# Kernel optimization log

Measured on AMD Instinct MI355X. Metric: run time of the kernel, lower is better.

Reference implementation:

```python
import jax, jax.numpy as jnp
import numpy as np

R = 0.2          # stable-distribution hash bucket width
TABLE_SIZE = 2   # hash table size (buckets)
M = 5            # number of appended ALSH transform dims
EPS = 1e-12


def conv2d(x, W, b, pad):
    out = jax.lax.conv_general_dilated(
        x, W, window_strides=(1, 1), padding=[(pad, pad), (pad, pad)],
        dimension_numbers=('NCHW', 'OIHW', 'NCHW'))
    return out + b[None, :, None, None]


def maxpool2(x):
    return jax.lax.reduce_window(x, -jnp.inf, jax.lax.max,
                                 (1, 1, 2, 2), (1, 1, 2, 2), 'VALID')


def alsh_mask(x, W, a, c):
    """ALSH filter selection: hash P(kernels) and Q(query) with a stable
    distribution hash h(v)=floor((a.v+b)/r) mod table_size; active filters
    are those landing in the query's bucket. Returns [B, Cout] 0/1 mask.
    Multiplying conv output by this mask == gather active filters then
    zero_fill_missing back to full channel count."""
    Cout, Cin, kH, kW = W.shape
    Kf = W.reshape(Cout, -1)                       # [Cout, Cin*kH*kW]
    norms = jnp.linalg.norm(Kf, axis=1)
    Kn = Kf / (jnp.max(norms) + EPS)               # scale so all norms <= 1
    n = jnp.linalg.norm(Kn, axis=1, keepdims=True)
    # P transform: append norm^2, norm^4, ..., norm^(2^M)
    powers = jnp.concatenate([n ** (2 ** (i + 1)) for i in range(M)], axis=1)
    P = jnp.concatenate([Kn, powers], axis=1)      # [Cout, d+M]
    kh = jnp.mod(jnp.floor((P @ a + c[0]) / R), TABLE_SIZE)  # [Cout]
    # query vector: per-sample channel means broadcast over kernel support
    cm = x.mean(axis=(2, 3))                       # [B, Cin]
    q = jnp.repeat(cm, kH * kW, axis=1)            # [B, Cin*kH*kW] (cin,kh,kw order)
    qn = q / (jnp.linalg.norm(q, axis=1, keepdims=True) + EPS)
    # Q transform: append M halves
    Qv = jnp.concatenate([qn, jnp.full((q.shape[0], M), 0.5, q.dtype)], axis=1)
    qh = jnp.mod(jnp.floor((Qv @ a + c[0]) / R), TABLE_SIZE)  # [B]
    return (kh[None, :] == qh[:, None]).astype(x.dtype)       # [B, Cout]


def setup_inputs() -> dict:
    key = jax.random.key(0)
    ks = jax.random.split(key, 16)
    u = lambda k, s: jax.random.uniform(k, s, jnp.float32, 0.0, R)
    n = lambda k, s, sc=0.1: jax.random.normal(k, s, jnp.float32) * sc
    return {
        'x': jax.random.normal(ks[0], (4096, 3, 32, 32), jnp.float32),
        'W1': n(ks[1], (16, 3, 5, 5)), 'b1': n(ks[2], (16,)),
        'a1': jax.random.normal(ks[3], (80,), jnp.float32), 'c1': u(ks[4], (1,)),
        'W2': n(ks[5], (20, 16, 5, 5)), 'b2': n(ks[6], (20,)),
        'a2': jax.random.normal(ks[7], (405,), jnp.float32), 'c2': u(ks[8], (1,)),
        'W3': n(ks[9], (20, 20, 5, 5)), 'b3': n(ks[10], (20,)),
        'a3': jax.random.normal(ks[11], (505,), jnp.float32), 'c3': u(ks[12], (1,)),
        'Wo': n(ks[13], (10, 320)), 'bo': n(ks[14], (10,)),
    }


def reference(x, W1, b1, a1, c1, W2, b2, a2, c2, W3, b3, a3, c3, Wo, bo):
    m1 = alsh_mask(x, W1, a1, c1)
    h = jax.nn.relu(conv2d(x, W1, b1, 2)) * m1[:, :, None, None]
    h = maxpool2(h)                                # [B,16,16,16]
    m2 = alsh_mask(h, W2, a2, c2)
    h = jax.nn.relu(conv2d(h, W2, b2, 2)) * m2[:, :, None, None]
    h = maxpool2(h)                                # [B,20,8,8]
    m3 = alsh_mask(h, W3, a3, c3)
    h = jax.nn.relu(conv2d(h, W3, b3, 2)) * m3[:, :, None, None]
    # zero_fill_missing -> identity here: inactive channels already zero
    h = maxpool2(h)                                # [B,20,4,4]
    flat = h.reshape(h.shape[0], -1)               # [B,320]
    return flat @ Wo.T + bo
```

## Files before the change

kernel.cpp:

```cpp
#include <hip/hip_runtime.h>
#include <hip/hip_bf16.h>

#define EPSV 1e-12
#define RHASH 0.2

__device__ __forceinline__ int fmod2(double t) {
    return (int)(((long long)floor(t)) & 1LL);
}

__device__ __forceinline__ void load_row6(const float* base, float* r) {
    float2 a0 = *(const float2*)(base);
    float2 a1 = *(const float2*)(base + 2);
    float2 a2 = *(const float2*)(base + 4);
    r[0] = a0.x; r[1] = a0.y; r[2] = a1.x; r[3] = a1.y; r[4] = a2.x; r[5] = a2.y;
}

__device__ __forceinline__ void load_row12(const float* base, float* r) {
    #pragma unroll
    for (int j = 0; j < 6; ++j) *(float2*)&r[2 * j] = *(const float2*)(base + 2 * j);
}

#define FMA4(c,kx,w) { float wg=(w); \
  acc[c][0]=fmaf(wg,cur[kx],acc[c][0]); acc[c][1]=fmaf(wg,cur[(kx)+1],acc[c][1]); \
  acc[c][2]=fmaf(wg,nxt[kx],acc[c][2]); acc[c][3]=fmaf(wg,nxt[(kx)+1],acc[c][3]); }

__device__ void layer_setup(const float* W, const float* a, double cval,
                            int Co, int Ci, int* kh, double* asum, double* qc,
                            double* s_norm, float* Wbuf, float* abuf)
{
    const int t = threadIdx.x;
    const int w = t >> 6, ln = t & 63;
    const int D = Ci * 25;
    for (int i = t; i < Co * D; i += 256) Wbuf[i] = W[i];
    for (int i = t; i < D + 5; i += 256) abuf[i] = a[i];
    __syncthreads();
    for (int co = w; co < Co; co += 4) {
        double s = 0;
        for (int j = ln; j < D; j += 64) { double x = (double)Wbuf[co * D + j]; s += x * x; }
        #pragma unroll
        for (int off = 32; off; off >>= 1) s += __shfl_xor(s, off);
        if (ln == 0) s_norm[co] = sqrt(s);
    }
    __syncthreads();
    if (t == 0) {
        double mx = 0;
        for (int i = 0; i < Co; ++i) mx = fmax(mx, s_norm[i]);
        s_norm[23] = 1.0 / (mx + EPSV);
    }
    __syncthreads();
    double scale = s_norm[23];
    for (int co = w; co < Co; co += 4) {
        double dp = 0;
        for (int j = ln; j < D; j += 64) dp += (double)Wbuf[co * D + j] * (double)abuf[j];
        #pragma unroll
        for (int off = 32; off; off >>= 1) dp += __shfl_xor(dp, off);
        if (ln == 0) {
            dp *= scale;
            double n = s_norm[co] * scale;
            double p = n * n;
            for (int m = 0; m < 5; ++m) { dp += p * (double)abuf[D + m]; p *= p; }
            kh[co] = fmod2((dp + cval) / RHASH);
        }
    }
    if (t >= 64 && t < 64 + Ci) {
        int c = t - 64;
        double s = 0;
        for (int j = 0; j < 25; ++j) s += (double)abuf[c * 25 + j];
        asum[c] = s;
    }
    if (t == 128) {
        double s = 0;
        for (int m = 0; m < 5; ++m) s += (double)abuf[D + m];
        *qc = 0.5 * s + cval;
    }
    __syncthreads();
}

__global__ __launch_bounds__(256) void prep_kernel(
    const float* W1, const float* a1, const float* c1,
    const float* W2, const float* a2, const float* c2,
    const float* W3, const float* a3, const float* c3,
    double* dmeta, int* imeta,
    float* Wp1, float* Wp2, float* Wp3)
{
    __shared__ float Wbuf[10000];
    __shared__ float abuf[512];
    __shared__ double s_norm[24];
    const int blk = blockIdx.x;
    if (blk == 0) {
        layer_setup(W1, a1, (double)c1[0], 16, 3,  imeta + 0,  dmeta + 0,  dmeta + 39, s_norm, Wbuf, abuf);
    } else if (blk == 1) {
        layer_setup(W2, a2, (double)c2[0], 20, 16, imeta + 16, dmeta + 3,  dmeta + 40, s_norm, Wbuf, abuf);
    } else if (blk == 2) {
        layer_setup(W3, a3, (double)c3[0], 20, 20, imeta + 36, dmeta + 19, dmeta + 41, s_norm, Wbuf, abuf);
    } else {
        int i = (blk - 3) * 256 + threadIdx.x;
        if (i < 1200) {
            int co = i & 15, r = i >> 4;
            int kx = r % 5, r2 = r / 5, ky = r2 % 5, ci = r2 / 5;
            Wp1[i] = W1[co * 75 + ci * 25 + ky * 5 + kx];
        } else if (i < 1200 + 8960) {
            int k = i - 1200;
            int j = k % 28, r = k / 28;
            int cog = r % 4, r2 = r / 4, ky = r2 % 5, ci = r2 / 5;
            Wp2[k] = (j < 25) ? W2[(cog * 5 + j / 5) * 400 + ci * 25 + ky * 5 + (j % 5)] : 0.f;
        } else if (i < 1200 + 8960 + 11200) {
            int k = i - 10160;
            int j = k % 28, r = k / 28;
            int cog = r % 4, r2 = r / 4, ky = r2 % 5, ci = r2 / 5;
            Wp3[k] = (j < 25) ? W3[(cog * 5 + j / 5) * 500 + ci * 25 + ky * 5 + (j % 5)] : 0.f;
        }
    }
}

__global__ __launch_bounds__(256) void conv1_kernel(
    const float* __restrict__ x, const float* __restrict__ Wp1,
    const float* __restrict__ b1, const int* __restrict__ kh1,
    const double* __restrict__ dmeta, float* __restrict__ h1,
    int* __restrict__ qh2)
{
    __shared__ float xs[3][36][38];
    __shared__ float Ws[1200];
    __shared__ double s_red[3][4];
    __shared__ double s_ch[16][4];

    const int b = blockIdx.x, t = threadIdx.x;
    const int w = t >> 6, ln = t & 63;

    for (int i = t; i < 3 * 36 * 38; i += 256) (&xs[0][0][0])[i] = 0.f;
    for (int i = t; i < 600; i += 256) ((float2*)Ws)[i] = ((const float2*)Wp1)[i];
    __syncthreads();

    const float2* xb2 = (const float2*)(x + (size_t)b * 3072);
    double psum[3] = {0, 0, 0};
    #pragma unroll
    for (int j = 0; j < 6; ++j) {
        int i = t + 256 * j;
        int rem = i & 511, row = rem >> 4, col2 = rem & 15;
        float2 v = xb2[i];
        *(float2*)&xs[j >> 1][row + 2][col2 * 2 + 2] = v;
        psum[j >> 1] += (double)v.x + (double)v.y;
    }
    #pragma unroll
    for (int c = 0; c < 3; ++c) {
        double s = psum[c];
        #pragma unroll
        for (int off = 32; off; off >>= 1) s += __shfl_xor(s, off);
        if (ln == 0) s_red[c][w] = s;
    }
    __syncthreads();

    double dp = 0, nn = 0;
    #pragma unroll
    for (int c = 0; c < 3; ++c) {
        double cm = (s_red[c][0] + s_red[c][1] + s_red[c][2] + s_red[c][3]) * (1.0 / 1024.0);
        dp += cm * dmeta[c]; nn += cm * cm;
    }
    const int qh = fmod2((dp / (5.0 * sqrt(nn) + EPSV) + dmeta[39]) / RHASH);

    const int cog = ln >> 4;
    const int py = 4 * w + ((ln >> 2) & 3), pxg = ln & 3;
    const int y0 = 2 * py, x0 = 8 * pxg;

    float accA[4][8], accB[4][8];
    #pragma unroll
    for (int c = 0; c < 4; ++c) {
        float bb = b1[cog * 4 + c];
        #pragma unroll
        for (int k = 0; k < 8; ++k) { accA[c][k] = bb; accB[c][k] = bb; }
    }

    #pragma unroll
    for (int ci = 0; ci < 3; ++ci) {
        float ra[12], rb[12];
        load_row12(&xs[ci][y0][x0],     ra);
        load_row12(&xs[ci][y0 + 1][x0], rb);
        #pragma unroll
        for (int ky = 0; ky < 5; ++ky) {
            const float4* wq = (const float4*)&Ws[((ci * 5 + ky) * 5) * 16 + cog * 4];
            #pragma unroll
            for (int kx = 0; kx < 5; ++kx) {
                float4 wv = wq[kx * 4];
                { float wg = wv.x;
                  #pragma unroll
                  for (int k = 0; k < 8; ++k) { accA[0][k] = fmaf(wg, ra[k + kx], accA[0][k]);
                                                accB[0][k] = fmaf(wg, rb[k + kx], accB[0][k]); } }
                { float wg = wv.y;
                  #pragma unroll
                  for (int k = 0; k < 8; ++k) { accA[1][k] = fmaf(wg, ra[k + kx], accA[1][k]);
                                                accB[1][k] = fmaf(wg, rb[k + kx], accB[1][k]); } }
                { float wg = wv.z;
                  #pragma unroll
                  for (int k = 0; k < 8; ++k) { accA[2][k] = fmaf(wg, ra[k + kx], accA[2][k]);
                                                accB[2][k] = fmaf(wg, rb[k + kx], accB[2][k]); } }
                { float wg = wv.w;
                  #pragma unroll
                  for (int k = 0; k < 8; ++k) { accA[3][k] = fmaf(wg, ra[k + kx], accA[3][k]);
                                                accB[3][k] = fmaf(wg, rb[k + kx], accB[3][k]); } }
            }
            if (ky < 4) {
                #pragma unroll
                for (int j = 0; j < 12; ++j) ra[j] = rb[j];
                load_row12(&xs[ci][y0 + ky + 2][x0], rb);
            }
        }
    }

    float* hb = h1 + (size_t)b * 4096 + py * 16 + pxg * 4;
    double csum[4];
    #pragma unroll
    for (int c = 0; c < 4; ++c) {
        int co = cog * 4 + c;
        float mask = (kh1[co] == qh) ? 1.f : 0.f;
        float v0 = fmaxf(fmaxf(accA[c][0], accA[c][1]), fmaxf(accB[c][0], accB[c][1]));
        float v1 = fmaxf(fmaxf(accA[c][2], accA[c][3]), fmaxf(accB[c][2], accB[c][3]));
        float v2 = fmaxf(fmaxf(accA[c][4], accA[c][5]), fmaxf(accB[c][4], accB[c][5]));
        float v3 = fmaxf(fmaxf(accA[c][6], accA[c][7]), fmaxf(accB[c][6], accB[c][7]));
        v0 = fmaxf(v0, 0.f) * mask; v1 = fmaxf(v1, 0.f) * mask;
        v2 = fmaxf(v2, 0.f) * mask; v3 = fmaxf(v3, 0.f) * mask;
        *(float4*)(hb + co * 256) = make_float4(v0, v1, v2, v3);
        csum[c] = (double)v0 + (double)v1 + (double)v2 + (double)v3;
    }
    #pragma unroll
    for (int c = 0; c < 4; ++c) {
        double s = csum[c];
        s += __shfl_xor(s, 8); s += __shfl_xor(s, 4);
        s += __shfl_xor(s, 2); s += __shfl_xor(s, 1);
        if ((ln & 15) == 0) s_ch[cog * 4 + c][w] = s;
    }
    __syncthreads();
    if (t == 0) {
        double dp2 = 0, nn2 = 0;
        #pragma unroll
        for (int c = 0; c < 16; ++c) {
            double cm = (s_ch[c][0] + s_ch[c][1] + s_ch[c][2] + s_ch[c][3]) * (1.0 / 256.0);
            dp2 += cm * dmeta[3 + c]; nn2 += cm * cm;
        }
        qh2[b] = fmod2((dp2 / (5.0 * sqrt(nn2) + EPSV) + dmeta[40]) / RHASH);
    }
}

#define C2_XLOAD(CH, RX) { \
    _Pragma("unroll") \
    for (int j = 0; j < 8; ++j) { \
        int i = t + 256 * j, si = i >> 9, rem = i & 511, cil = rem >> 7, rr = rem & 127; \
        RX[j] = (b0 + si < B) ? ((const float2*)h1)[(size_t)(b0 + si) * 2048 + ((CH) * 4 + cil) * 128 + rr] \
                              : make_float2(0.f, 0.f); \
    } }

#define C2_XCOMMIT(RX) { \
    _Pragma("unroll") \
    for (int j = 0; j < 8; ++j) { \
        int i = t + 256 * j, si = i >> 9, rem = i & 511, cil = rem >> 7, rr = rem & 127; \
        int p2 = rr * 2, row = p2 >> 4, col = p2 & 15; \
        *(float2*)&xs[si][cil][row + 2][col + 2] = RX[j]; \
    } }

__global__ __launch_bounds__(256) void conv2_kernel(
    const float* __restrict__ h1, const float* __restrict__ Wp2,
    const float* __restrict__ b2, const int* __restrict__ kh2,
    const int* __restrict__ qh2, const double* __restrict__ dmeta,
    float* __restrict__ h2, int* __restrict__ qh3, int B)
{
    __shared__ float xs[4][4][20][22];
    __shared__ float Ws[2240];
    __shared__ double s_ch[4][20];

    const int b0 = blockIdx.x * 4, t = threadIdx.x;
    const int s = t >> 6, l = t & 63;
    const int cog = l >> 4, pos = l & 15;
    const int py = pos >> 1, pxg = pos & 1;
    const int b = b0 + s;

    for (int i = t; i < 4 * 4 * 20 * 22; i += 256) (&xs[0][0][0][0])[i] = 0.f;

    const int qh = (b < B) ? qh2[b] : 0;
    float accA[5][8], accB[5][8];
    #pragma unroll
    for (int c = 0; c < 5; ++c) {
        float bb = b2[cog * 5 + c];
        #pragma unroll
        for (int k = 0; k < 8; ++k) { accA[c][k] = bb; accB[c][k] = bb; }
    }

    float2 rx[8];
    C2_XLOAD(0, rx);
    __syncthreads();

    for (int ch = 0; ch < 4; ++ch) {
        for (int i = t; i < 1120; i += 256)
            ((float2*)Ws)[i] = ((const float2*)(Wp2 + ch * 2240))[i];
        C2_XCOMMIT(rx);
        __syncthreads();
        if (ch < 3) C2_XLOAD(ch + 1, rx);

        for (int cil = 0; cil < 4; ++cil) {
            float ra[12], rb[12];
            load_row12(&xs[s][cil][2 * py][8 * pxg],     ra);
            load_row12(&xs[s][cil][2 * py + 1][8 * pxg], rb);
            #pragma unroll
            for (int ky = 0; ky < 5; ++ky) {
                float wv[28];
                const float4* wp = (const float4*)&Ws[((cil * 5 + ky) * 4 + cog) * 28];
                *(float4*)&wv[0]  = wp[0];
                *(float4*)&wv[4]  = wp[1];
                *(float4*)&wv[8]  = wp[2];
                *(float4*)&wv[12] = wp[3];
                *(float4*)&wv[16] = wp[4];
                *(float4*)&wv[20] = wp[5];
                *(float4*)&wv[24] = wp[6];
                #pragma unroll
                for (int c = 0; c < 5; ++c) {
                    #pragma unroll
                    for (int kx = 0; kx < 5; ++kx) {
                        float wg = wv[c * 5 + kx];
                        #pragma unroll
                        for (int k = 0; k < 8; ++k) {
                            accA[c][k] = fmaf(wg, ra[k + kx], accA[c][k]);
                            accB[c][k] = fmaf(wg, rb[k + kx], accB[c][k]);
                        }
                    }
                }
                if (ky < 4) {
                    #pragma unroll
                    for (int j = 0; j < 12; ++j) ra[j] = rb[j];
                    load_row12(&xs[s][cil][2 * py + ky + 2][8 * pxg], rb);
                }
            }
        }
        __syncthreads();
    }

    float* ob = h2 + (size_t)b * 1280 + py * 8 + pxg * 4;
    double csum[5];
    #pragma unroll
    for (int c = 0; c < 5; ++c) {
        int co = cog * 5 + c;
        float mask = (kh2[co] == qh) ? 1.f : 0.f;
        float v0 = fmaxf(fmaxf(accA[c][0], accA[c][1]), fmaxf(accB[c][0], accB[c][1]));
        float v1 = fmaxf(fmaxf(accA[c][2], accA[c][3]), fmaxf(accB[c][2], accB[c][3]));
        float v2 = fmaxf(fmaxf(accA[c][4], accA[c][5]), fmaxf(accB[c][4], accB[c][5]));
        float v3 = fmaxf(fmaxf(accA[c][6], accA[c][7]), fmaxf(accB[c][6], accB[c][7]));
        v0 = fmaxf(v0, 0.f) * mask; v1 = fmaxf(v1, 0.f) * mask;
        v2 = fmaxf(v2, 0.f) * mask; v3 = fmaxf(v3, 0.f) * mask;
        if (b < B) *(float4*)(ob + co * 64) = make_float4(v0, v1, v2, v3);
        csum[c] = (double)v0 + (double)v1 + (double)v2 + (double)v3;
    }
    #pragma unroll
    for (int c = 0; c < 5; ++c) {
        double sv = csum[c];
        sv += __shfl_xor(sv, 8); sv += __shfl_xor(sv, 4);
        sv += __shfl_xor(sv, 2); sv += __shfl_xor(sv, 1);
        if (pos == 0) s_ch[s][cog * 5 + c] = sv;
    }
    __syncthreads();
    if (l == 0 && b < B) {
        double dp2 = 0, nn2 = 0;
        #pragma unroll
        for (int c = 0; c < 20; ++c) {
            double cm = s_ch[s][c] * (1.0 / 64.0);
            dp2 += cm * dmeta[19 + c]; nn2 += cm * cm;
        }
        qh3[b] = fmod2((dp2 / (5.0 * sqrt(nn2) + EPSV) + dmeta[41]) / RHASH);
    }
}

#define C3_WLOAD(CH, RW) { \
    _Pragma("unroll") \
    for (int j = 0; j < 6; ++j) { \
        int i = t + 256 * j; \
        if (i < 1400) RW[j] = ((const float2*)(Wp3 + (CH) * 2800))[i]; \
    } }

#define C3_WCOMMIT(RW) { \
    _Pragma("unroll") \
    for (int j = 0; j < 6; ++j) { \
        int i = t + 256 * j; \
        if (i < 1400) ((float2*)Ws)[i] = RW[j]; \
    } }

#define C3_XLOAD(CH, RX) { \
    _Pragma("unroll") \
    for (int j = 0; j < 3; ++j) { \
        int i = t + 256 * j; \
        if (i < 640) { \
            int ss = i / 160, r = i - ss * 160, ci = r >> 5, rr = r & 31; \
            RX[j] = (b0 + ss < B) ? ((const float2*)(h2 + (size_t)(b0 + ss) * 1280 + ((CH) * 5 + ci) * 64))[rr] \
                                  : make_float2(0.f, 0.f); \
        } \
    } }

#define C3_XCOMMIT(RX) { \
    _Pragma("unroll") \
    for (int j = 0; j < 3; ++j) { \
        int i = t + 256 * j; \
        if (i < 640) { \
            int ss = i / 160, r = i - ss * 160, ci = r >> 5, rr = r & 31, p2 = rr * 2; \
            *(float2*)&xs[ss][ci][(p2 >> 3) + 2][(p2 & 7) + 2] = RX[j]; \
        } \
    } }

__global__ __launch_bounds__(256) void conv3_kernel(
    const float* __restrict__ h2, const float* __restrict__ Wp3,
    const float* __restrict__ b3, const int* __restrict__ kh3,
    const int* __restrict__ qh3,
    const float* __restrict__ Wo, const float* __restrict__ bo,
    float* __restrict__ out, int B)
{
    __shared__ float xs[4][5][12][12];
    __shared__ float Ws[2800];
    __shared__ float flat[4][320];

    const int b0 = blockIdx.x * 4, t = threadIdx.x;
    const int s = t >> 6, q0 = t & 63, cog = q0 >> 4, pos = q0 & 15;
    const int py = pos >> 2, px = pos & 3;
    const int y0 = 2 * py, x0 = 2 * px;
    const int b = b0 + s;

    for (int i = t; i < 4 * 5 * 144; i += 256) (&xs[0][0][0][0])[i] = 0.f;

    const int qh = (b < B) ? qh3[b] : 0;
    float acc[5][4];
    #pragma unroll
    for (int c = 0; c < 5; ++c) {
        float bb = b3[cog * 5 + c];
        acc[c][0] = bb; acc[c][1] = bb; acc[c][2] = bb; acc[c][3] = bb;
    }

    float2 rw[6], rx[3];
    C3_WLOAD(0, rw);
    C3_XLOAD(0, rx);

    for (int ch = 0; ch < 4; ++ch) {
        C3_WCOMMIT(rw);
        C3_XCOMMIT(rx);
        __syncthreads();
        if (ch < 3) { C3_WLOAD(ch + 1, rw); C3_XLOAD(ch + 1, rx); }

        #pragma unroll
        for (int ci = 0; ci < 5; ++ci) {
            float cur[6], nxt[6];
            load_row6(&xs[s][ci][y0][x0], cur);
            load_row6(&xs[s][ci][y0 + 1][x0], nxt);
            #pragma unroll
            for (int ky = 0; ky < 5; ++ky) {
                const float* wrow = &Ws[((ci * 5 + ky) * 4 + cog) * 28];
                const float4* wq = (const float4*)wrow;
                float4 q;
                q = wq[0]; FMA4(0, 0, q.x) FMA4(0, 1, q.y) FMA4(0, 2, q.z) FMA4(0, 3, q.w)
                q = wq[1]; FMA4(0, 4, q.x) FMA4(1, 0, q.y) FMA4(1, 1, q.z) FMA4(1, 2, q.w)
                q = wq[2]; FMA4(1, 3, q.x) FMA4(1, 4, q.y) FMA4(2, 0, q.z) FMA4(2, 1, q.w)
                q = wq[3]; FMA4(2, 2, q.x) FMA4(2, 3, q.y) FMA4(2, 4, q.z) FMA4(3, 0, q.w)
                q = wq[4]; FMA4(3, 1, q.x) FMA4(3, 2, q.y) FMA4(3, 3, q.z) FMA4(3, 4, q.w)
                q = wq[5]; FMA4(4, 0, q.x) FMA4(4, 1, q.y) FMA4(4, 2, q.z) FMA4(4, 3, q.w)
                FMA4(4, 4, wrow[24])
                if (ky < 4) {
                    #pragma unroll
                    for (int j = 0; j < 6; ++j) cur[j] = nxt[j];
                    load_row6(&xs[s][ci][y0 + ky + 2][x0], nxt);
                }
            }
        }
        __syncthreads();
    }

    #pragma unroll
    for (int c = 0; c < 5; ++c) {
        int co = cog * 5 + c;
        float m = fmaxf(fmaxf(acc[c][0], acc[c][1]), fmaxf(acc[c][2], acc[c][3]));
        flat[s][co * 16 + pos] = fmaxf(m, 0.f) * ((kh3[co] == qh) ? 1.f : 0.f);
    }
    __syncthreads();

    if (t < 160) {
        const int g = t >> 2, qq = t & 3;
        const int ss = g / 10, o = g - ss * 10;
        float a = 0.f;
        const float* wr = Wo + o * 320;
        for (int k = qq; k < 320; k += 4) a = fmaf(flat[ss][k], wr[k], a);
        a += __shfl_xor(a, 1);
        a += __shfl_xor(a, 2);
        if (qq == 0 && b0 + ss < B) out[(size_t)(b0 + ss) * 10 + o] = a + bo[o];
    }
}

extern "C" void kernel_launch(void* const* d_in, const int* in_sizes, int n_in,
                              void* d_out, int out_size, void* d_ws, size_t ws_size,
                              hipStream_t stream)
{
    const float* x  = (const float*)d_in[0];
    const float* W1 = (const float*)d_in[1];
    const float* b1 = (const float*)d_in[2];
    const float* a1 = (const float*)d_in[3];
    const float* c1 = (const float*)d_in[4];
    const float* W2 = (const float*)d_in[5];
    const float* b2 = (const float*)d_in[6];
    const float* a2 = (const float*)d_in[7];
    const float* c2 = (const float*)d_in[8];
    const float* W3 = (const float*)d_in[9];
    const float* b3 = (const float*)d_in[10];
    const float* a3 = (const float*)d_in[11];
    const float* c3 = (const float*)d_in[12];
    const float* Wo = (const float*)d_in[13];
    const float* bo = (const float*)d_in[14];
    float* out = (float*)d_out;

    const int B = in_sizes[0] / 3072;

    float* h1  = (float*)d_ws;
    float* h2  = h1 + (size_t)B * 4096;
    float* Wp1 = h2 + (size_t)B * 1280;
    float* Wp2 = Wp1 + 1200;
    float* Wp3 = Wp2 + 8960;
    double* dmeta = (double*)(Wp3 + 11200);
    int* imeta = (int*)(dmeta + 42);
    int* qh2 = imeta + 56;
    int* qh3 = qh2 + B;

    prep_kernel<<<87, 256, 0, stream>>>(W1, a1, c1, W2, a2, c2, W3, a3, c3,
                                        dmeta, imeta, Wp1, Wp2, Wp3);
    conv1_kernel<<<B, 256, 0, stream>>>(x, Wp1, b1, imeta, dmeta, h1, qh2);
    conv2_kernel<<<(B + 3) / 4, 256, 0, stream>>>(h1, Wp2, b2, imeta + 16, qh2, dmeta, h2, qh3, B);
    conv3_kernel<<<(B + 3) / 4, 256, 0, stream>>>(h2, Wp3, b3, imeta + 36, qh3, Wo, bo, out, B);
}
```

Before: 468.9 us.

## Widen conv3 to 8 samples per block and zero only padding halos

conv3 now runs 512 threads per block on 8 samples. Each weight chunk loaded to shared memory is reused across twice as many samples, and input channels are staged in 2 chunks of 10 instead of 4 chunks of 5, so there are fewer sync rounds. The flat buffer reuses the xs shared memory, and both conv1 and conv3 write zeros only to the halo border instead of clearing the whole tile. conv1 also issues its global input loads before the weight copy so their latency overlaps. The larger shared footprint (about 68KB) and 512-thread blocks may lower occupancy and halve the number of conv3 blocks.

```diff
diff --git a/kernel.cpp b/kernel.cpp
--- a/kernel.cpp
+++ b/kernel.cpp
@@ -127,19 +127,27 @@
     const int b = blockIdx.x, t = threadIdx.x;
     const int w = t >> 6, ln = t & 63;
 
-    for (int i = t; i < 3 * 36 * 38; i += 256) (&xs[0][0][0])[i] = 0.f;
+    const float2* xb2 = (const float2*)(x + (size_t)b * 3072);
+    float2 rxv[6];
+    #pragma unroll
+    for (int j = 0; j < 6; ++j) rxv[j] = xb2[t + 256 * j];
+
     for (int i = t; i < 600; i += 256) ((float2*)Ws)[i] = ((const float2*)Wp1)[i];
-    __syncthreads();
-
-    const float2* xb2 = (const float2*)(x + (size_t)b * 3072);
+
+    for (int i = t; i < 1032; i += 256) {
+        int ci = i / 344, r = i - ci * 344;
+        int row, col;
+        if (r < 152) { int rr = r / 38; col = r - rr * 38; row = (rr < 2) ? rr : rr + 32; }
+        else { int q = r - 152; row = 2 + q / 6; int cq = q - (q / 6) * 6; col = (cq < 2) ? cq : cq + 32; }
+        xs[ci][row][col] = 0.f;
+    }
+
     double psum[3] = {0, 0, 0};
     #pragma unroll
     for (int j = 0; j < 6; ++j) {
-        int i = t + 256 * j;
-        int rem = i & 511, row = rem >> 4, col2 = rem & 15;
-        float2 v = xb2[i];
-        *(float2*)&xs[j >> 1][row + 2][col2 * 2 + 2] = v;
-        psum[j >> 1] += (double)v.x + (double)v.y;
+        int i = t + 256 * j, rem = i & 511, row = rem >> 4, col2 = rem & 15;
+        *(float2*)&xs[j >> 1][row + 2][col2 * 2 + 2] = rxv[j];
+        psum[j >> 1] += (double)rxv[j].x + (double)rxv[j].y;
     }
     #pragma unroll
     for (int c = 0; c < 3; ++c) {
@@ -365,60 +373,78 @@
     }
 }
 
-#define C3_WLOAD(CH, RW) { \
+#define C3B_WLOAD(CH, RW) { \
     _Pragma("unroll") \
     for (int j = 0; j < 6; ++j) { \
-        int i = t + 256 * j; \
-        if (i < 1400) RW[j] = ((const float2*)(Wp3 + (CH) * 2800))[i]; \
-    } }
-
-#define C3_WCOMMIT(RW) { \
+        int i = t + 512 * j; \
+        if (i < 2800) RW[j] = ((const float2*)(Wp3 + (CH) * 5600))[i]; \
+    } }
+
+#define C3B_WCOMMIT(RW) { \
     _Pragma("unroll") \
     for (int j = 0; j < 6; ++j) { \
-        int i = t + 256 * j; \
-        if (i < 1400) ((float2*)Ws)[i] = RW[j]; \
-    } }
-
-#define C3_XLOAD(CH, RX) { \
+        int i = t + 512 * j; \
+        if (i < 2800) ((float2*)Ws)[i] = RW[j]; \
+    } }
+
+#define C3B_XLOAD(CH, RX) { \
     _Pragma("unroll") \
-    for (int j = 0; j < 3; ++j) { \
-        int i = t + 256 * j; \
-        if (i < 640) { \
-            int ss = i / 160, r = i - ss * 160, ci = r >> 5, rr = r & 31; \
-            RX[j] = (b0 + ss < B) ? ((const float2*)(h2 + (size_t)(b0 + ss) * 1280 + ((CH) * 5 + ci) * 64))[rr] \
-                                  : make_float2(0.f, 0.f); \
+    for (int j = 0; j < 5; ++j) { \
+        int i = t + 512 * j; \
+        int ss = i / 320, r = i - ss * 320, ci = r >> 5, rr = r & 31; \
+        RX[j] = (b0 + ss < B) ? ((const float2*)(h2 + (size_t)(b0 + ss) * 1280 + ((CH) * 10 + ci) * 64))[rr] \
+                              : make_float2(0.f, 0.f); \
+    } }
+
+#define C3B_XCOMMIT(RX) { \
+    _Pragma("unroll") \
+    for (int j = 0; j < 5; ++j) { \
+        int i = t + 512 * j; \
+        int ss = i / 320, r = i - ss * 320, ci = r >> 5, rr = r & 31, p2 = rr * 2; \
+        *(float2*)&xs[ss][ci][(p2 >> 3) + 2][(p2 & 7) + 2] = RX[j]; \
+    } }
+
+#define C3B_COMPUTE { \
+    for (int ci = 0; ci < 10; ++ci) { \
+        float cur[6], nxt[6]; \
+        load_row6(&xs[s][ci][y0][x0], cur); \
+        load_row6(&xs[s][ci][y0 + 1][x0], nxt); \
+        _Pragma("unroll") \
+        for (int ky = 0; ky < 5; ++ky) { \
+            const float* wrow = &Ws[((ci * 5 + ky) * 4 + cog) * 28]; \
+            const float4* wq = (const float4*)wrow; \
+            float4 q; \
+            q = wq[0]; FMA4(0, 0, q.x) FMA4(0, 1, q.y) FMA4(0, 2, q.z) FMA4(0, 3, q.w) \
+            q = wq[1]; FMA4(0, 4, q.x) FMA4(1, 0, q.y) FMA4(1, 1, q.z) FMA4(1, 2, q.w) \
+            q = wq[2]; FMA4(1, 3, q.x) FMA4(1, 4, q.y) FMA4(2, 0, q.z) FMA4(2, 1, q.w) \
+            q = wq[3]; FMA4(2, 2, q.x) FMA4(2, 3, q.y) FMA4(2, 4, q.z) FMA4(3, 0, q.w) \
+            q = wq[4]; FMA4(3, 1, q.x) FMA4(3, 2, q.y) FMA4(3, 3, q.z) FMA4(3, 4, q.w) \
+            q = wq[5]; FMA4(4, 0, q.x) FMA4(4, 1, q.y) FMA4(4, 2, q.z) FMA4(4, 3, q.w) \
+            FMA4(4, 4, wrow[24]) \
+            if (ky < 4) { \
+                _Pragma("unroll") \
+                for (int j = 0; j < 6; ++j) cur[j] = nxt[j]; \
+                load_row6(&xs[s][ci][y0 + ky + 2][x0], nxt); \
+            } \
         } \
     } }
 
-#define C3_XCOMMIT(RX) { \
-    _Pragma("unroll") \
-    for (int j = 0; j < 3; ++j) { \
-        int i = t + 256 * j; \
-        if (i < 640) { \
-            int ss = i / 160, r = i - ss * 160, ci = r >> 5, rr = r & 31, p2 = rr * 2; \
-            *(float2*)&xs[ss][ci][(p2 >> 3) + 2][(p2 & 7) + 2] = RX[j]; \
-        } \
-    } }
-
-__global__ __launch_bounds__(256) void conv3_kernel(
+__global__ __launch_bounds__(512) void conv3_kernel(
     const float* __restrict__ h2, const float* __restrict__ Wp3,
     const float* __restrict__ b3, const int* __restrict__ kh3,
     const int* __restrict__ qh3,
     const float* __restrict__ Wo, const float* __restrict__ bo,
     float* __restrict__ out, int B)
 {
-    __shared__ float xs[4][5][12][12];
-    __shared__ float Ws[2800];
-    __shared__ float flat[4][320];
-
-    const int b0 = blockIdx.x * 4, t = threadIdx.x;
+    __shared__ float xs[8][10][12][12];
+    __shared__ float Ws[5600];
+
+    const int b0 = blockIdx.x * 8, t = threadIdx.x;
     const int s = t >> 6, q0 = t & 63, cog = q0 >> 4, pos = q0 & 15;
     const int py = pos >> 2, px = pos & 3;
     const int y0 = 2 * py, x0 = 2 * px;
     const int b = b0 + s;
 
-    for (int i = t; i < 4 * 5 * 144; i += 256) (&xs[0][0][0][0])[i] = 0.f;
-
     const int qh = (b < B) ? qh3[b] : 0;
     float acc[5][4];
     #pragma unroll
@@ -427,57 +453,47 @@
         acc[c][0] = bb; acc[c][1] = bb; acc[c][2] = bb; acc[c][3] = bb;
     }
 
-    float2 rw[6], rx[3];
-    C3_WLOAD(0, rw);
-    C3_XLOAD(0, rx);
-
-    for (int ch = 0; ch < 4; ++ch) {
-        C3_WCOMMIT(rw);
-        C3_XCOMMIT(rx);
-        __syncthreads();
-        if (ch < 3) { C3_WLOAD(ch + 1, rw); C3_XLOAD(ch + 1, rx); }
-
-        #pragma unroll
-        for (int ci = 0; ci < 5; ++ci) {
-            float cur[6], nxt[6];
-            load_row6(&xs[s][ci][y0][x0], cur);
-            load_row6(&xs[s][ci][y0 + 1][x0], nxt);
-            #pragma unroll
-            for (int ky = 0; ky < 5; ++ky) {
-                const float* wrow = &Ws[((ci * 5 + ky) * 4 + cog) * 28];
-                const float4* wq = (const float4*)wrow;
-                float4 q;
-                q = wq[0]; FMA4(0, 0, q.x) FMA4(0, 1, q.y) FMA4(0, 2, q.z) FMA4(0, 3, q.w)
-                q = wq[1]; FMA4(0, 4, q.x) FMA4(1, 0, q.y) FMA4(1, 1, q.z) FMA4(1, 2, q.w)
-                q = wq[2]; FMA4(1, 3, q.x) FMA4(1, 4, q.y) FMA4(2, 0, q.z) FMA4(2, 1, q.w)
-                q = wq[3]; FMA4(2, 2, q.x) FMA4(2, 3, q.y) FMA4(2, 4, q.z) FMA4(3, 0, q.w)
-                q = wq[4]; FMA4(3, 1, q.x) FMA4(3, 2, q.y) FMA4(3, 3, q.z) FMA4(3, 4, q.w)
-                q = wq[5]; FMA4(4, 0, q.x) FMA4(4, 1, q.y) FMA4(4, 2, q.z) FMA4(4, 3, q.w)
-                FMA4(4, 4, wrow[24])
-                if (ky < 4) {
-                    #pragma unroll
-                    for (int j = 0; j < 6; ++j) cur[j] = nxt[j];
-                    load_row6(&xs[s][ci][y0 + ky + 2][x0], nxt);
-                }
-            }
-        }
-        __syncthreads();
-    }
-
+    float2 rw[6], rx[5];
+    C3B_WLOAD(0, rw);
+    C3B_XLOAD(0, rx);
+
+    for (int i = t; i < 6400; i += 512) {
+        int tile = i / 80, r = i - tile * 80;
+        int ss = tile / 10, ci = tile - ss * 10;
+        int row, col;
+        if (r < 48) { int rr = r / 12; col = r - rr * 12; row = (rr < 2) ? rr : rr + 8; }
+        else { int q = r - 48; row = 2 + (q >> 2); int cq = q & 3; col = (cq < 2) ? cq : cq + 8; }
+        xs[ss][ci][row][col] = 0.f;
+    }
+    C3B_WCOMMIT(rw);
+    C3B_XCOMMIT(rx);
+    __syncthreads();
+
+    C3B_WLOAD(1, rw);
+    C3B_XLOAD(1, rx);
+    C3B_COMPUTE
+    __syncthreads();
+    C3B_WCOMMIT(rw);
+    C3B_XCOMMIT(rx);
+    __syncthreads();
+    C3B_COMPUTE
+    __syncthreads();
+
+    float* flat = &xs[0][0][0][0];
     #pragma unroll
     for (int c = 0; c < 5; ++c) {
         int co = cog * 5 + c;
         float m = fmaxf(fmaxf(acc[c][0], acc[c][1]), fmaxf(acc[c][2], acc[c][3]));
-        flat[s][co * 16 + pos] = fmaxf(m, 0.f) * ((kh3[co] == qh) ? 1.f : 0.f);
-    }
-    __syncthreads();
-
-    if (t < 160) {
+        flat[s * 320 + co * 16 + pos] = fmaxf(m, 0.f) * ((kh3[co] == qh) ? 1.f : 0.f);
+    }
+    __syncthreads();
+
+    if (t < 320) {
         const int g = t >> 2, qq = t & 3;
         const int ss = g / 10, o = g - ss * 10;
         float a = 0.f;
         const float* wr = Wo + o * 320;
-        for (int k = qq; k < 320; k += 4) a = fmaf(flat[ss][k], wr[k], a);
+        for (int k = qq; k < 320; k += 4) a = fmaf(flat[ss * 320 + k], wr[k], a);
         a += __shfl_xor(a, 1);
         a += __shfl_xor(a, 2);
         if (qq == 0 && b0 + ss < B) out[(size_t)(b0 + ss) * 10 + o] = a + bo[o];
@@ -521,5 +537,5 @@
                                         dmeta, imeta, Wp1, Wp2, Wp3);
     conv1_kernel<<<B, 256, 0, stream>>>(x, Wp1, b1, imeta, dmeta, h1, qh2);
     conv2_kernel<<<(B + 3) / 4, 256, 0, stream>>>(h1, Wp2, b2, imeta + 16, qh2, dmeta, h2, qh3, B);
-    conv3_kernel<<<(B + 3) / 4, 256, 0, stream>>>(h2, Wp3, b3, imeta + 36, qh3, Wo, bo, out, B);
-}
+    conv3_kernel<<<(B + 7) / 8, 512, 0, stream>>>(h2, Wp3, b3, imeta + 36, qh3, Wo, bo, out, B);
+}
```

Result: no change. 473.7 us (+1.0%).
